# Performance work log

Measured on AMD Instinct MI355X. Metric: run time of the kernel, lower is better.

The kernel has to match this reference:

```python
import jax, jax.numpy as jnp
import numpy as np

KERNEL = 8


def setup_inputs() -> dict:
    key = jax.random.key(0)
    ks = jax.random.split(key, 9)
    N, Cin, L = 16, 128, 2048
    Cout = 256
    x = jax.random.normal(ks[0], (N, Cin, L), dtype=jnp.float32)
    conv_w = jax.random.normal(ks[1], (Cout, Cin, KERNEL), dtype=jnp.float32) * (1.0 / np.sqrt(Cin * KERNEL))
    conv_b = jax.random.normal(ks[2], (Cout,), dtype=jnp.float32) * 0.01
    wq = jax.random.normal(ks[3], (Cout, Cout), dtype=jnp.float32) * (1.0 / np.sqrt(Cout))
    bq = jax.random.normal(ks[4], (Cout,), dtype=jnp.float32) * 0.01
    wk = jax.random.normal(ks[5], (Cout, Cout), dtype=jnp.float32) * (1.0 / np.sqrt(Cout))
    bk = jax.random.normal(ks[6], (Cout,), dtype=jnp.float32) * 0.01
    wv = jax.random.normal(ks[7], (Cout, Cout), dtype=jnp.float32) * (1.0 / np.sqrt(Cout))
    bv = jax.random.normal(ks[8], (Cout,), dtype=jnp.float32) * 0.01
    return {"x": x, "conv_w": conv_w, "conv_b": conv_b,
            "wq": wq, "bq": bq, "wk": wk, "bk": bk, "wv": wv, "bv": bv}


def reference(x, conv_w, conv_b, wq, bq, wk, bk, wv, bv):
    # Conv1d, valid padding: [N, Cin, L] -> [N, Cout, S], S = L - KERNEL + 1
    h = jax.lax.conv_general_dilated(
        x, conv_w, window_strides=(1,), padding='VALID',
        dimension_numbers=('NCH', 'OIH', 'NCH'))
    h = jax.nn.relu(h + conv_b[None, :, None])
    N, C, S = h.shape
    h = jnp.transpose(h, (0, 2, 1))  # [N, S, C]
    # Linear layers (torch convention: y = x @ W^T + b)
    q = jnp.einsum('nsc,dc->nsd', h, wq) + bq
    k = jnp.einsum('nsc,dc->nsd', h, wk) + bk
    v = jnp.einsum('nsc,dc->nsd', h, wv) + bv
    # sigmoid (non-normalized) attention over full SxS scores
    scores = jnp.einsum('nsd,ntd->nst', q, k) / jnp.sqrt(jnp.asarray(C, h.dtype))
    attn = jax.nn.sigmoid(scores)  # [N, S, S]
    out = jnp.einsum('nst,ntd->nsd', attn, v)
    return jnp.transpose(out, (0, 2, 1))  # [N, C, S]
```

## Files before the change

kernel.cpp:

```cpp
#include <hip/hip_runtime.h>

typedef short short8 __attribute__((ext_vector_type(8)));
typedef float f32x4 __attribute__((ext_vector_type(4)));
typedef float f32x16 __attribute__((ext_vector_type(16)));
typedef unsigned short u16x4 __attribute__((ext_vector_type(4)));

constexpr int NB = 16, CIN = 128, LIN = 2048, CO = 256;
constexpr int SL = 2041;
constexpr int MT = NB * SL;
constexpr int MP = 32768;
constexpr int XTS = 136;

constexpr size_t XT_OFF = 0;
constexpr size_t XT_SZ  = (size_t)NB*LIN*XTS*2 + 65536;
constexpr size_t CW_OFF = XT_OFF + XT_SZ;
constexpr size_t CW_SZ  = (size_t)CO*CIN*8*2;
constexpr size_t WQ_OFF = CW_OFF + CW_SZ;
constexpr size_t WB_SZ  = (size_t)CO*CO*2;
constexpr size_t WK_OFF = WQ_OFF + WB_SZ;
constexpr size_t WV_OFF = WK_OFF + WB_SZ;
constexpr size_t H_OFF  = WV_OFF + WB_SZ;
constexpr size_t HB_SZ  = (size_t)MP*CO*2;
constexpr size_t Q_OFF  = H_OFF + HB_SZ;
constexpr size_t K_OFF  = Q_OFF + HB_SZ;
constexpr size_t VT_OFF = K_OFF + HB_SZ;

__device__ inline unsigned short f2bf(float f) {
  union { float f; unsigned int u; } v; v.f = f;
  unsigned int r = v.u + 0x7fffu + ((v.u >> 16) & 1u);
  return (unsigned short)(r >> 16);
}

#if defined(__has_builtin)
#if __has_builtin(__builtin_amdgcn_global_load_lds)
#define HAVE_GLDS 1
#endif
#endif

__device__ inline void gld16(const unsigned short* g, void* l) {
#ifdef HAVE_GLDS
  __builtin_amdgcn_global_load_lds(
      (const __attribute__((address_space(1))) void*)g,
      (__attribute__((address_space(3))) void*)l, 16, 0, 0);
#else
  *(short8*)l = *(const short8*)g;
#endif
}

__global__ void xpose_kernel(const float* __restrict__ x, unsigned short* __restrict__ xt) {
  __shared__ float tile[32][33];
  const int tx = threadIdx.x, ty = threadIdx.y;
  const int s0 = blockIdx.x * 32, c0 = blockIdx.y * 32, n = blockIdx.z;
  #pragma unroll
  for (int r = 0; r < 4; ++r)
    tile[ty * 4 + r][tx] = x[((size_t)(n * CIN + c0 + ty * 4 + r)) * LIN + s0 + tx];
  __syncthreads();
  #pragma unroll
  for (int r = 0; r < 4; ++r)
    xt[((size_t)(n * LIN + s0 + ty * 4 + r)) * XTS + c0 + tx] = f2bf(tile[tx][ty * 4 + r]);
}

__global__ void wconv_kernel(const float* __restrict__ w, unsigned short* __restrict__ o) {
  int idx = blockIdx.x * 256 + threadIdx.x;
  int co = idx >> 10, r = idx & 1023, kp = r >> 7, ci = r & 127;
  o[idx] = f2bf(w[co * 1024 + ci * 8 + kp]);
}

__global__ void wqkv_kernel(const float* __restrict__ a, const float* __restrict__ b,
                            const float* __restrict__ c, unsigned short* __restrict__ oa,
                            unsigned short* __restrict__ ob, unsigned short* __restrict__ oc) {
  int z = blockIdx.x >> 6, lb = blockIdx.x & 63;
  const float* src = (z == 0) ? a : (z == 1) ? b : c;
  unsigned short* dst = (z == 0) ? oa : (z == 1) ? ob : oc;
  int i = (lb * 256 + threadIdx.x) * 4;
  float4 v = *(const float4*)(src + i);
  u16x4 r;
  r.x = f2bf(v.x); r.y = f2bf(v.y); r.z = f2bf(v.z); r.w = f2bf(v.w);
  *(u16x4*)(dst + i) = r;
}

__global__ __launch_bounds__(256) void conv_gemm(
    const unsigned short* __restrict__ xt,
    const unsigned short* __restrict__ wb,
    const float* __restrict__ bias,
    unsigned short* __restrict__ h)
{
  __shared__ unsigned short sX[18432];
  __shared__ unsigned short sB[4096];
  const int tid = threadIdx.x;
  const int w = tid >> 6, lane = tid & 63, quad = lane >> 4, l16 = lane & 15;
  const int n  = blockIdx.y;
  const int s0 = blockIdx.x * 128;
  const int d0 = blockIdx.z * 128;

  {
    const unsigned short* xbase = xt + ((size_t)n * LIN + s0) * XTS;
    #pragma unroll
    for (int i = 0; i < 9; ++i) {
      int u = i * 256 + tid;
      gld16(xbase + u * 8, ((char*)sX) + u * 16);
    }
  }

  f32x4 acc[2][8];
  #pragma unroll
  for (int i = 0; i < 2; ++i)
    #pragma unroll
    for (int j = 0; j < 8; ++j) acc[i][j] = (f32x4){0.f, 0.f, 0.f, 0.f};

  for (int kc = 0; kc < 32; ++kc) {
    const int kp = kc >> 2, ci0 = (kc & 3) * 32;
    __syncthreads();
    #pragma unroll
    for (int i2 = 0; i2 < 2; ++i2) {
      int off = (i2 * 256 + tid) * 16;
      int row = off >> 6, kgs = (off >> 4) & 3;
      int kg = kgs ^ ((row >> 1) & 3);
      gld16(wb + (size_t)(d0 + row) * 1024 + kp * 128 + ci0 + kg * 8, ((char*)sB) + off);
    }
    __syncthreads();

    short8 bfr[8];
    #pragma unroll
    for (int j = 0; j < 8; ++j) {
      int r = j * 16 + l16;
      bfr[j] = *(const short8*)(sB + r * 32 + (quad ^ ((r >> 1) & 3)) * 8);
    }

    #pragma unroll
    for (int i = 0; i < 2; ++i) {
      int srow = w * 32 + i * 16 + l16;
      short8 afr = *(const short8*)(sX + (srow + kp) * XTS + ci0 + quad * 8);
      #pragma unroll
      for (int j = 0; j < 8; ++j)
        acc[i][j] = __builtin_amdgcn_mfma_f32_16x16x32_bf16(afr, bfr[j], acc[i][j], 0, 0, 0);
    }
  }

  #pragma unroll
  for (int i = 0; i < 2; ++i)
    #pragma unroll
    for (int j = 0; j < 8; ++j) {
      int col = d0 + j * 16 + l16;
      float bv = bias[col];
      #pragma unroll
      for (int jj = 0; jj < 4; ++jj) {
        int s = s0 + w * 32 + i * 16 + quad * 4 + jj;
        if (s < SL) {
          float val = fmaxf(acc[i][j][jj] + bv, 0.f);
          h[(size_t)(n * SL + s) * CO + col] = f2bf(val);
        }
      }
    }
}

__global__ __launch_bounds__(256) void lin_gemm(
    const unsigned short* __restrict__ A,
    const unsigned short* __restrict__ Bq, const unsigned short* __restrict__ Bk,
    const unsigned short* __restrict__ Bv,
    const float* __restrict__ biq, const float* __restrict__ bik,
    const float* __restrict__ biv,
    unsigned short* __restrict__ qb, unsigned short* __restrict__ kb,
    unsigned short* __restrict__ vtb)
{
  __shared__ unsigned short sA[4096];
  __shared__ unsigned short sB[4096];
  const int tid = threadIdx.x;
  const int w = tid >> 6, lane = tid & 63, quad = lane >> 4, l16 = lane & 15;
  const int m0 = blockIdx.x * 128, d0 = blockIdx.y * 128, z = blockIdx.z;
  const unsigned short* B = (z == 0) ? Bq : (z == 1) ? Bk : Bv;
  const float* bias        = (z == 0) ? biq : (z == 1) ? bik : biv;

  f32x4 acc[2][8];
  #pragma unroll
  for (int i = 0; i < 2; ++i)
    #pragma unroll
    for (int j = 0; j < 8; ++j) acc[i][j] = (f32x4){0.f, 0.f, 0.f, 0.f};

  for (int kc = 0; kc < 8; ++kc) {
    __syncthreads();
    #pragma unroll
    for (int i2 = 0; i2 < 2; ++i2) {
      int off = (i2 * 256 + tid) * 16;
      int row = off >> 6, kgs = (off >> 4) & 3;
      int kg = kgs ^ ((row >> 1) & 3);
      gld16(A + (size_t)(m0 + row) * CO + kc * 32 + kg * 8, ((char*)sA) + off);
      gld16(B + (size_t)(d0 + row) * CO + kc * 32 + kg * 8, ((char*)sB) + off);
    }
    __syncthreads();

    short8 afr[2], bfr[8];
    #pragma unroll
    for (int i = 0; i < 2; ++i) {
      int r = w * 32 + i * 16 + l16;
      afr[i] = *(const short8*)(sA + r * 32 + (quad ^ ((r >> 1) & 3)) * 8);
    }
    #pragma unroll
    for (int j = 0; j < 8; ++j) {
      int r = j * 16 + l16;
      bfr[j] = *(const short8*)(sB + r * 32 + (quad ^ ((r >> 1) & 3)) * 8);
    }
    #pragma unroll
    for (int i = 0; i < 2; ++i)
      #pragma unroll
      for (int j = 0; j < 8; ++j)
        acc[i][j] = __builtin_amdgcn_mfma_f32_16x16x32_bf16(afr[i], bfr[j], acc[i][j], 0, 0, 0);
  }

  #pragma unroll
  for (int i = 0; i < 2; ++i)
    #pragma unroll
    for (int j = 0; j < 8; ++j) {
      int col = d0 + j * 16 + l16;
      float bv = bias[col];
      #pragma unroll
      for (int jj = 0; jj < 4; ++jj) {
        int m = m0 + w * 32 + i * 16 + quad * 4 + jj;
        float val = acc[i][j][jj] + bv;
        if (z < 2) {
          ((z == 0) ? qb : kb)[(size_t)m * CO + col] = f2bf(val);
        } else if (m < MT) {
          int nn = m / SL, ss = m - nn * SL;
          vtb[(size_t)col * MP + nn * 2048 + ss] = f2bf(val);
        }
      }
    }
}

__global__ __launch_bounds__(256) void attn_kernel(
    const unsigned short* __restrict__ qb,
    const unsigned short* __restrict__ kb,
    const unsigned short* __restrict__ vtb,
    float* __restrict__ out)
{
  __shared__ char smem[40960];
  unsigned short* sKV = (unsigned short*)smem;
  unsigned short* sP  = (unsigned short*)(smem + 32768);
  const int tid = threadIdx.x;
  const int w = tid >> 6, lane = tid & 63;
  const int half = lane >> 5, l32 = lane & 31;
  const int n = blockIdx.y, s0 = blockIdx.x * 64;
  const int mi = w & 1, wh = w >> 1;

  short8 qf[16];
  {
    const unsigned short* qp =
        qb + (size_t)(n * SL + s0 + mi * 32 + l32) * CO + half * 8;
    #pragma unroll
    for (int kk = 0; kk < 16; ++kk) qf[kk] = *(const short8*)(qp + kk * 16);
  }

  f32x16 o[4];
  #pragma unroll
  for (int di = 0; di < 4; ++di)
    #pragma unroll
    for (int r = 0; r < 16; ++r) o[di][r] = 0.f;

  for (int t0 = 0; t0 < 2048; t0 += 64) {
    __syncthreads();
    #pragma unroll
    for (int i = 0; i < 8; ++i) {
      int u = i * 256 + tid;
      int trow = u >> 5, slot = u & 31;
      gld16(kb + (size_t)(n * SL + t0 + trow) * CO + (slot ^ (trow & 31)) * 8,
            ((char*)sKV) + u * 16);
    }
    __syncthreads();

    f32x16 sacc;
    #pragma unroll
    for (int r = 0; r < 16; ++r) sacc[r] = 0.f;
    const int tl = wh * 32 + l32;
    #pragma unroll
    for (int kk = 0; kk < 16; ++kk) {
      int g = kk * 2 + half;
      short8 kf = *(const short8*)(sKV + tl * 256 + (g ^ (tl & 31)) * 8);
      sacc = __builtin_amdgcn_mfma_f32_32x32x16_bf16(qf[kk], kf, sacc, 0, 0, 0);
    }

    #pragma unroll
    for (int r = 0; r < 16; ++r) {
      int srow = mi * 32 + (r & 3) + 8 * (r >> 2) + 4 * half;
      float p = 1.f / (1.f + __expf(-sacc[r] * 0.0625f));
      sP[srow * 64 + (((tl >> 3) ^ (srow & 7)) << 3) + (tl & 7)] =
          (t0 + tl < SL) ? f2bf(p) : (unsigned short)0;
    }
    __syncthreads();

    #pragma unroll
    for (int i = 0; i < 8; ++i) {
      int u = i * 256 + tid;
      int drow = u >> 3, slot = u & 7;
      gld16(vtb + (size_t)drow * MP + n * 2048 + t0 + (slot ^ (drow & 7)) * 8,
            ((char*)sKV) + u * 16);
    }
    __syncthreads();

    #pragma unroll
    for (int kt = 0; kt < 4; ++kt) {
      int gc = kt * 2 + half;
      int srow = mi * 32 + l32;
      short8 pa = *(const short8*)(sP + srow * 64 + ((gc ^ (srow & 7)) << 3));
      #pragma unroll
      for (int di = 0; di < 4; ++di) {
        int d = (wh * 4 + di) * 32 + l32;
        short8 vf = *(const short8*)(sKV + d * 64 + ((gc ^ (d & 7)) << 3));
        o[di] = __builtin_amdgcn_mfma_f32_32x32x16_bf16(pa, vf, o[di], 0, 0, 0);
      }
    }
  }

  #pragma unroll
  for (int di = 0; di < 4; ++di) {
    int d = (wh * 4 + di) * 32 + l32;
    float* op = out + (size_t)n * CO * SL + (size_t)d * SL;
    #pragma unroll
    for (int r = 0; r < 16; ++r) {
      int s = s0 + mi * 32 + (r & 3) + 8 * (r >> 2) + 4 * half;
      if (s < SL) op[s] = o[di][r];
    }
  }
}

extern "C" void kernel_launch(void* const* d_in, const int* in_sizes, int n_in,
                              void* d_out, int out_size, void* d_ws, size_t ws_size,
                              hipStream_t stream) {
  const float* x      = (const float*)d_in[0];
  const float* conv_w = (const float*)d_in[1];
  const float* conv_b = (const float*)d_in[2];
  const float* wq     = (const float*)d_in[3];
  const float* bq     = (const float*)d_in[4];
  const float* wk     = (const float*)d_in[5];
  const float* bk     = (const float*)d_in[6];
  const float* wv     = (const float*)d_in[7];
  const float* bv     = (const float*)d_in[8];

  char* ws = (char*)d_ws;
  unsigned short* xt  = (unsigned short*)(ws + XT_OFF);
  unsigned short* cw  = (unsigned short*)(ws + CW_OFF);
  unsigned short* wqb = (unsigned short*)(ws + WQ_OFF);
  unsigned short* wkb = (unsigned short*)(ws + WK_OFF);
  unsigned short* wvb = (unsigned short*)(ws + WV_OFF);
  unsigned short* hb  = (unsigned short*)(ws + H_OFF);
  unsigned short* qb  = (unsigned short*)(ws + Q_OFF);
  unsigned short* kb  = (unsigned short*)(ws + K_OFF);
  unsigned short* vtb = (unsigned short*)(ws + VT_OFF);

  hipLaunchKernelGGL(xpose_kernel, dim3(64, 4, 16), dim3(32, 8), 0, stream, x, xt);
  hipLaunchKernelGGL(wconv_kernel, dim3(1024), dim3(256), 0, stream, conv_w, cw);
  hipLaunchKernelGGL(wqkv_kernel,  dim3(192), dim3(256), 0, stream,
                     wq, wk, wv, wqb, wkb, wvb);
  hipLaunchKernelGGL(conv_gemm, dim3(16, 16, 2), dim3(256), 0, stream, xt, cw, conv_b, hb);
  hipLaunchKernelGGL(lin_gemm,  dim3(256, 2, 3), dim3(256), 0, stream,
                     hb, wqb, wkb, wvb, bq, bk, bv, qb, kb, vtb);
  hipLaunchKernelGGL(attn_kernel, dim3(32, 16), dim3(256), 0, stream,
                     qb, kb, vtb, (float*)d_out);
}
```

Baseline: 286.9 us.

## Restructure attention to 32-row tiles reading K and V directly from global

The attention kernel now processes 32 query rows per block instead of 64, with each wave computing its own 32 key columns of a 128-wide key tile. K and V fragments are loaded straight from global memory rather than staged through shared memory, so only the probability tile stays in LDS, and one of the two barriers per step is removed. The grid doubles and launch bounds request 4 blocks per CU to raise occupancy. The cost is no reuse of K/V across waves in LDS, so global and L2 traffic rises, including strided V loads.

```diff
diff --git a/kernel.cpp b/kernel.cpp
--- a/kernel.cpp
+++ b/kernel.cpp
@@ -227,97 +227,77 @@
     }
 }
 
-__global__ __launch_bounds__(256) void attn_kernel(
+__global__ __launch_bounds__(256, 4) void attn_kernel(
     const unsigned short* __restrict__ qb,
     const unsigned short* __restrict__ kb,
     const unsigned short* __restrict__ vtb,
     float* __restrict__ out)
 {
-  __shared__ char smem[40960];
-  unsigned short* sKV = (unsigned short*)smem;
-  unsigned short* sP  = (unsigned short*)(smem + 32768);
+  __shared__ unsigned short sP[32 * 128];
   const int tid = threadIdx.x;
   const int w = tid >> 6, lane = tid & 63;
   const int half = lane >> 5, l32 = lane & 31;
-  const int n = blockIdx.y, s0 = blockIdx.x * 64;
-  const int mi = w & 1, wh = w >> 1;
+  const int n = blockIdx.y, s0 = blockIdx.x * 32;
+  const int tl = w * 32 + l32;
 
   short8 qf[16];
   {
-    const unsigned short* qp =
-        qb + (size_t)(n * SL + s0 + mi * 32 + l32) * CO + half * 8;
+    const unsigned short* qp = qb + (size_t)(n * SL + s0 + l32) * CO + half * 8;
     #pragma unroll
     for (int kk = 0; kk < 16; ++kk) qf[kk] = *(const short8*)(qp + kk * 16);
   }
 
-  f32x16 o[4];
-  #pragma unroll
-  for (int di = 0; di < 4; ++di)
-    #pragma unroll
-    for (int r = 0; r < 16; ++r) o[di][r] = 0.f;
-
-  for (int t0 = 0; t0 < 2048; t0 += 64) {
-    __syncthreads();
-    #pragma unroll
-    for (int i = 0; i < 8; ++i) {
-      int u = i * 256 + tid;
-      int trow = u >> 5, slot = u & 31;
-      gld16(kb + (size_t)(n * SL + t0 + trow) * CO + (slot ^ (trow & 31)) * 8,
-            ((char*)sKV) + u * 16);
-    }
-    __syncthreads();
-
+  f32x16 o[2];
+  #pragma unroll
+  for (int dd = 0; dd < 2; ++dd)
+    #pragma unroll
+    for (int r = 0; r < 16; ++r) o[dd][r] = 0.f;
+
+  const unsigned short* kbase = kb + (size_t)(n * SL) * CO + half * 8;
+  const unsigned short* vbase = vtb + (size_t)n * 2048;
+
+  for (int t0 = 0; t0 < 2048; t0 += 128) {
+    const unsigned short* kp = kbase + (size_t)(t0 + tl) * CO;
     f32x16 sacc;
     #pragma unroll
     for (int r = 0; r < 16; ++r) sacc[r] = 0.f;
-    const int tl = wh * 32 + l32;
     #pragma unroll
     for (int kk = 0; kk < 16; ++kk) {
-      int g = kk * 2 + half;
-      short8 kf = *(const short8*)(sKV + tl * 256 + (g ^ (tl & 31)) * 8);
+      short8 kf = *(const short8*)(kp + kk * 16);
       sacc = __builtin_amdgcn_mfma_f32_32x32x16_bf16(qf[kk], kf, sacc, 0, 0, 0);
     }
 
+    __syncthreads();
     #pragma unroll
     for (int r = 0; r < 16; ++r) {
-      int srow = mi * 32 + (r & 3) + 8 * (r >> 2) + 4 * half;
+      int srow = (r & 3) + 8 * (r >> 2) + 4 * half;
       float p = 1.f / (1.f + __expf(-sacc[r] * 0.0625f));
-      sP[srow * 64 + (((tl >> 3) ^ (srow & 7)) << 3) + (tl & 7)] =
+      sP[srow * 128 + (((tl >> 3) ^ (srow & 15)) << 3) + (tl & 7)] =
           (t0 + tl < SL) ? f2bf(p) : (unsigned short)0;
     }
     __syncthreads();
 
     #pragma unroll
-    for (int i = 0; i < 8; ++i) {
-      int u = i * 256 + tid;
-      int drow = u >> 3, slot = u & 7;
-      gld16(vtb + (size_t)drow * MP + n * 2048 + t0 + (slot ^ (drow & 7)) * 8,
-            ((char*)sKV) + u * 16);
-    }
-    __syncthreads();
-
-    #pragma unroll
-    for (int kt = 0; kt < 4; ++kt) {
-      int gc = kt * 2 + half;
-      int srow = mi * 32 + l32;
-      short8 pa = *(const short8*)(sP + srow * 64 + ((gc ^ (srow & 7)) << 3));
-      #pragma unroll
-      for (int di = 0; di < 4; ++di) {
-        int d = (wh * 4 + di) * 32 + l32;
-        short8 vf = *(const short8*)(sKV + d * 64 + ((gc ^ (d & 7)) << 3));
-        o[di] = __builtin_amdgcn_mfma_f32_32x32x16_bf16(pa, vf, o[di], 0, 0, 0);
+    for (int kt = 0; kt < 8; ++kt) {
+      int g = kt * 2 + half;
+      short8 pa = *(const short8*)(sP + l32 * 128 + ((g ^ (l32 & 15)) << 3));
+      #pragma unroll
+      for (int dd = 0; dd < 2; ++dd) {
+        int d = (w * 2 + dd) * 32 + l32;
+        short8 vf = *(const short8*)(vbase + (size_t)d * MP + t0 + g * 8);
+        o[dd] = __builtin_amdgcn_mfma_f32_32x32x16_bf16(pa, vf, o[dd], 0, 0, 0);
       }
     }
   }
 
   #pragma unroll
-  for (int di = 0; di < 4; ++di) {
-    int d = (wh * 4 + di) * 32 + l32;
+  for (int dd = 0; dd < 2; ++dd) {
+    int d = (w * 2 + dd) * 32 + l32;
     float* op = out + (size_t)n * CO * SL + (size_t)d * SL;
     #pragma unroll
     for (int r = 0; r < 16; ++r) {
-      int s = s0 + mi * 32 + (r & 3) + 8 * (r >> 2) + 4 * half;
-      if (s < SL) op[s] = o[di][r];
+      int s = s0 + (r & 3) + 8 * (r >> 2) + 4 * half;
+      if (s < SL) op[s] = o[dd][r];
     }
   }
 }
@@ -353,6 +333,6 @@
   hipLaunchKernelGGL(conv_gemm, dim3(16, 16, 2), dim3(256), 0, stream, xt, cw, conv_b, hb);
   hipLaunchKernelGGL(lin_gemm,  dim3(256, 2, 3), dim3(256), 0, stream,
                      hb, wqb, wkb, wvb, bq, bk, bv, qb, kb, vtb);
-  hipLaunchKernelGGL(attn_kernel, dim3(32, 16), dim3(256), 0, stream,
+  hipLaunchKernelGGL(attn_kernel, dim3(64, 16), dim3(256), 0, stream,
                      qb, kb, vtb, (float*)d_out);
 }
```

Measured after the change: 488.6 us. 70.3% more time.

## Prefetch next tiles into registers with double-buffered LDS across GEMM and attention

Applied to the files above, without the earlier changes.

Replaces the direct global-to-LDS loads in conv_gemm, lin_gemm and attn_kernel with register prefetch of the next K/V or weight tile, issued before the current tile's MFMA work and written to LDS afterwards. The GEMMs double-buffer LDS so each k-step needs one barrier instead of two. Attention keeps separate K and V buffers, so it no longer reloads V after the scores, and it remaps the grid to a 1D index that groups batches, with launch_bounds(256,2). The cost is higher register pressure (attention holds 16 extra short8 registers on top of qf and the accumulators), and a custom waitcnt barrier replaces __syncthreads.

```diff
diff --git a/kernel.cpp b/kernel.cpp
--- a/kernel.cpp
+++ b/kernel.cpp
@@ -31,6 +31,13 @@
   return (unsigned short)(r >> 16);
 }
 
+__device__ inline void sync_lds() {
+  __asm__ volatile("" ::: "memory");
+  __builtin_amdgcn_s_waitcnt(0xc07f);
+  __builtin_amdgcn_s_barrier();
+  __asm__ volatile("" ::: "memory");
+}
+
 #if defined(__has_builtin)
 #if __has_builtin(__builtin_amdgcn_global_load_lds)
 #define HAVE_GLDS 1
@@ -86,7 +93,7 @@
     unsigned short* __restrict__ h)
 {
   __shared__ unsigned short sX[18432];
-  __shared__ unsigned short sB[4096];
+  __shared__ unsigned short sB[2][4096];
   const int tid = threadIdx.x;
   const int w = tid >> 6, lane = tid & 63, quad = lane >> 4, l16 = lane & 15;
   const int n  = blockIdx.y;
@@ -102,6 +109,19 @@
     }
   }
 
+  const int brow0 = tid >> 2, bkgs = tid & 3;
+  short8 breg[2];
+  #pragma unroll
+  for (int i2 = 0; i2 < 2; ++i2) {
+    int row = i2 * 64 + brow0;
+    int kg = bkgs ^ ((row >> 1) & 3);
+    breg[i2] = *(const short8*)(wb + (size_t)(d0 + row) * 1024 + 0 * 128 + 0 + kg * 8);
+  }
+  #pragma unroll
+  for (int i2 = 0; i2 < 2; ++i2)
+    *(short8*)(&sB[0][(i2 * 256 + tid) * 8]) = breg[i2];
+  __syncthreads();
+
   f32x4 acc[2][8];
   #pragma unroll
   for (int i = 0; i < 2; ++i)
@@ -109,24 +129,23 @@
     for (int j = 0; j < 8; ++j) acc[i][j] = (f32x4){0.f, 0.f, 0.f, 0.f};
 
   for (int kc = 0; kc < 32; ++kc) {
+    const int kcn = (kc < 31) ? kc + 1 : kc;
+    const int kpn = kcn >> 2, ci0n = (kcn & 3) * 32;
+    #pragma unroll
+    for (int i2 = 0; i2 < 2; ++i2) {
+      int row = i2 * 64 + brow0;
+      int kg = bkgs ^ ((row >> 1) & 3);
+      breg[i2] = *(const short8*)(wb + (size_t)(d0 + row) * 1024 + kpn * 128 + ci0n + kg * 8);
+    }
+
     const int kp = kc >> 2, ci0 = (kc & 3) * 32;
-    __syncthreads();
-    #pragma unroll
-    for (int i2 = 0; i2 < 2; ++i2) {
-      int off = (i2 * 256 + tid) * 16;
-      int row = off >> 6, kgs = (off >> 4) & 3;
-      int kg = kgs ^ ((row >> 1) & 3);
-      gld16(wb + (size_t)(d0 + row) * 1024 + kp * 128 + ci0 + kg * 8, ((char*)sB) + off);
-    }
-    __syncthreads();
-
+    const unsigned short* sBc = sB[kc & 1];
     short8 bfr[8];
     #pragma unroll
     for (int j = 0; j < 8; ++j) {
       int r = j * 16 + l16;
-      bfr[j] = *(const short8*)(sB + r * 32 + (quad ^ ((r >> 1) & 3)) * 8);
-    }
-
+      bfr[j] = *(const short8*)(sBc + r * 32 + (quad ^ ((r >> 1) & 3)) * 8);
+    }
     #pragma unroll
     for (int i = 0; i < 2; ++i) {
       int srow = w * 32 + i * 16 + l16;
@@ -135,6 +154,11 @@
       for (int j = 0; j < 8; ++j)
         acc[i][j] = __builtin_amdgcn_mfma_f32_16x16x32_bf16(afr, bfr[j], acc[i][j], 0, 0, 0);
     }
+
+    #pragma unroll
+    for (int i2 = 0; i2 < 2; ++i2)
+      *(short8*)(&sB[(kc + 1) & 1][(i2 * 256 + tid) * 8]) = breg[i2];
+    sync_lds();
   }
 
   #pragma unroll
@@ -163,14 +187,30 @@
     unsigned short* __restrict__ qb, unsigned short* __restrict__ kb,
     unsigned short* __restrict__ vtb)
 {
-  __shared__ unsigned short sA[4096];
-  __shared__ unsigned short sB[4096];
+  __shared__ unsigned short sA[2][4096];
+  __shared__ unsigned short sB[2][4096];
   const int tid = threadIdx.x;
   const int w = tid >> 6, lane = tid & 63, quad = lane >> 4, l16 = lane & 15;
   const int m0 = blockIdx.x * 128, d0 = blockIdx.y * 128, z = blockIdx.z;
   const unsigned short* B = (z == 0) ? Bq : (z == 1) ? Bk : Bv;
   const float* bias        = (z == 0) ? biq : (z == 1) ? bik : biv;
 
+  const int brow0 = tid >> 2, bkgs = tid & 3;
+  short8 areg[2], breg[2];
+  #pragma unroll
+  for (int i2 = 0; i2 < 2; ++i2) {
+    int row = i2 * 64 + brow0;
+    int kg = bkgs ^ ((row >> 1) & 3);
+    areg[i2] = *(const short8*)(A + (size_t)(m0 + row) * CO + kg * 8);
+    breg[i2] = *(const short8*)(B + (size_t)(d0 + row) * CO + kg * 8);
+  }
+  #pragma unroll
+  for (int i2 = 0; i2 < 2; ++i2) {
+    *(short8*)(&sA[0][(i2 * 256 + tid) * 8]) = areg[i2];
+    *(short8*)(&sB[0][(i2 * 256 + tid) * 8]) = breg[i2];
+  }
+  sync_lds();
+
   f32x4 acc[2][8];
   #pragma unroll
   for (int i = 0; i < 2; ++i)
@@ -178,33 +218,40 @@
     for (int j = 0; j < 8; ++j) acc[i][j] = (f32x4){0.f, 0.f, 0.f, 0.f};
 
   for (int kc = 0; kc < 8; ++kc) {
-    __syncthreads();
+    const int kcn = (kc < 7) ? kc + 1 : kc;
     #pragma unroll
     for (int i2 = 0; i2 < 2; ++i2) {
-      int off = (i2 * 256 + tid) * 16;
-      int row = off >> 6, kgs = (off >> 4) & 3;
-      int kg = kgs ^ ((row >> 1) & 3);
-      gld16(A + (size_t)(m0 + row) * CO + kc * 32 + kg * 8, ((char*)sA) + off);
-      gld16(B + (size_t)(d0 + row) * CO + kc * 32 + kg * 8, ((char*)sB) + off);
-    }
-    __syncthreads();
-
+      int row = i2 * 64 + brow0;
+      int kg = bkgs ^ ((row >> 1) & 3);
+      areg[i2] = *(const short8*)(A + (size_t)(m0 + row) * CO + kcn * 32 + kg * 8);
+      breg[i2] = *(const short8*)(B + (size_t)(d0 + row) * CO + kcn * 32 + kg * 8);
+    }
+
+    const unsigned short* sAc = sA[kc & 1];
+    const unsigned short* sBc = sB[kc & 1];
     short8 afr[2], bfr[8];
     #pragma unroll
     for (int i = 0; i < 2; ++i) {
       int r = w * 32 + i * 16 + l16;
-      afr[i] = *(const short8*)(sA + r * 32 + (quad ^ ((r >> 1) & 3)) * 8);
+      afr[i] = *(const short8*)(sAc + r * 32 + (quad ^ ((r >> 1) & 3)) * 8);
     }
     #pragma unroll
     for (int j = 0; j < 8; ++j) {
       int r = j * 16 + l16;
-      bfr[j] = *(const short8*)(sB + r * 32 + (quad ^ ((r >> 1) & 3)) * 8);
+      bfr[j] = *(const short8*)(sBc + r * 32 + (quad ^ ((r >> 1) & 3)) * 8);
     }
     #pragma unroll
     for (int i = 0; i < 2; ++i)
       #pragma unroll
       for (int j = 0; j < 8; ++j)
         acc[i][j] = __builtin_amdgcn_mfma_f32_16x16x32_bf16(afr[i], bfr[j], acc[i][j], 0, 0, 0);
+
+    #pragma unroll
+    for (int i2 = 0; i2 < 2; ++i2) {
+      *(short8*)(&sA[(kc + 1) & 1][(i2 * 256 + tid) * 8]) = areg[i2];
+      *(short8*)(&sB[(kc + 1) & 1][(i2 * 256 + tid) * 8]) = breg[i2];
+    }
+    sync_lds();
   }
 
   #pragma unroll
@@ -227,54 +274,75 @@
     }
 }
 
-__global__ __launch_bounds__(256) void attn_kernel(
+__global__ __launch_bounds__(256, 2) void attn_kernel(
     const unsigned short* __restrict__ qb,
     const unsigned short* __restrict__ kb,
     const unsigned short* __restrict__ vtb,
     float* __restrict__ out)
 {
-  __shared__ char smem[40960];
-  unsigned short* sKV = (unsigned short*)smem;
-  unsigned short* sP  = (unsigned short*)(smem + 32768);
+  __shared__ unsigned short sK[16384];
+  __shared__ unsigned short sV[16384];
+  __shared__ unsigned short sP[4096];
   const int tid = threadIdx.x;
   const int w = tid >> 6, lane = tid & 63;
   const int half = lane >> 5, l32 = lane & 31;
-  const int n = blockIdx.y, s0 = blockIdx.x * 64;
+  const int bidx = blockIdx.x;
+  const int n = (bidx & 7) + ((bidx >> 8) << 3);
+  const int s0 = ((bidx >> 3) & 31) * 64;
   const int mi = w & 1, wh = w >> 1;
+  const int tl = wh * 32 + l32;
+
+  const int ktrow = tid >> 5, kslot = tid & 31;
+  const int vdrow = tid >> 3, vslot = tid & 7;
 
   short8 qf[16];
   {
-    const unsigned short* qp =
-        qb + (size_t)(n * SL + s0 + mi * 32 + l32) * CO + half * 8;
+    const unsigned short* qp = qb + (size_t)(n * SL + s0 + mi * 32 + l32) * CO + half * 8;
     #pragma unroll
     for (int kk = 0; kk < 16; ++kk) qf[kk] = *(const short8*)(qp + kk * 16);
   }
 
+  const unsigned short* kbN = kb + (size_t)(n * SL) * CO;
+  const unsigned short* vbN = vtb + (size_t)n * 2048;
+
+  short8 kreg[8], vreg[8];
+  #pragma unroll
+  for (int i = 0; i < 8; ++i) {
+    int trow = i * 8 + ktrow;
+    kreg[i] = *(const short8*)(kbN + (size_t)trow * CO + ((kslot ^ (trow & 31)) << 3));
+    int drow = i * 32 + vdrow;
+    vreg[i] = *(const short8*)(vbN + (size_t)drow * MP + ((vslot ^ (drow & 7)) << 3));
+  }
+  #pragma unroll
+  for (int i = 0; i < 8; ++i) {
+    *(short8*)(sK + (i * 256 + tid) * 8) = kreg[i];
+    *(short8*)(sV + (i * 256 + tid) * 8) = vreg[i];
+  }
+  sync_lds();
+
   f32x16 o[4];
   #pragma unroll
   for (int di = 0; di < 4; ++di)
     #pragma unroll
     for (int r = 0; r < 16; ++r) o[di][r] = 0.f;
 
-  for (int t0 = 0; t0 < 2048; t0 += 64) {
-    __syncthreads();
+  for (int it = 0; it < 32; ++it) {
+    const int t0 = it * 64;
+    const int tn = (it < 31) ? t0 + 64 : t0;
     #pragma unroll
     for (int i = 0; i < 8; ++i) {
-      int u = i * 256 + tid;
-      int trow = u >> 5, slot = u & 31;
-      gld16(kb + (size_t)(n * SL + t0 + trow) * CO + (slot ^ (trow & 31)) * 8,
-            ((char*)sKV) + u * 16);
-    }
-    __syncthreads();
+      int trow = i * 8 + ktrow;
+      kreg[i] = *(const short8*)(kbN + (size_t)(tn + trow) * CO + ((kslot ^ (trow & 31)) << 3));
+      int drow = i * 32 + vdrow;
+      vreg[i] = *(const short8*)(vbN + (size_t)drow * MP + tn + ((vslot ^ (drow & 7)) << 3));
+    }
 
     f32x16 sacc;
     #pragma unroll
     for (int r = 0; r < 16; ++r) sacc[r] = 0.f;
-    const int tl = wh * 32 + l32;
     #pragma unroll
     for (int kk = 0; kk < 16; ++kk) {
-      int g = kk * 2 + half;
-      short8 kf = *(const short8*)(sKV + tl * 256 + (g ^ (tl & 31)) * 8);
+      short8 kf = *(const short8*)(sK + tl * 256 + (((kk * 2 + half) ^ (tl & 31)) << 3));
       sacc = __builtin_amdgcn_mfma_f32_32x32x16_bf16(qf[kk], kf, sacc, 0, 0, 0);
     }
 
@@ -285,29 +353,28 @@
       sP[srow * 64 + (((tl >> 3) ^ (srow & 7)) << 3) + (tl & 7)] =
           (t0 + tl < SL) ? f2bf(p) : (unsigned short)0;
     }
-    __syncthreads();
-
-    #pragma unroll
-    for (int i = 0; i < 8; ++i) {
-      int u = i * 256 + tid;
-      int drow = u >> 3, slot = u & 7;
-      gld16(vtb + (size_t)drow * MP + n * 2048 + t0 + (slot ^ (drow & 7)) * 8,
-            ((char*)sKV) + u * 16);
-    }
-    __syncthreads();
+    sync_lds();
 
     #pragma unroll
     for (int kt = 0; kt < 4; ++kt) {
-      int gc = kt * 2 + half;
+      int g2 = kt * 2 + half;
       int srow = mi * 32 + l32;
-      short8 pa = *(const short8*)(sP + srow * 64 + ((gc ^ (srow & 7)) << 3));
+      short8 pa = *(const short8*)(sP + srow * 64 + ((g2 ^ (srow & 7)) << 3));
       #pragma unroll
       for (int di = 0; di < 4; ++di) {
         int d = (wh * 4 + di) * 32 + l32;
-        short8 vf = *(const short8*)(sKV + d * 64 + ((gc ^ (d & 7)) << 3));
+        short8 vf = *(const short8*)(sV + d * 64 + ((g2 ^ (d & 7)) << 3));
         o[di] = __builtin_amdgcn_mfma_f32_32x32x16_bf16(pa, vf, o[di], 0, 0, 0);
       }
     }
+    sync_lds();
+
+    #pragma unroll
+    for (int i = 0; i < 8; ++i) {
+      *(short8*)(sK + (i * 256 + tid) * 8) = kreg[i];
+      *(short8*)(sV + (i * 256 + tid) * 8) = vreg[i];
+    }
+    sync_lds();
   }
 
   #pragma unroll
@@ -353,6 +420,6 @@
   hipLaunchKernelGGL(conv_gemm, dim3(16, 16, 2), dim3(256), 0, stream, xt, cw, conv_b, hb);
   hipLaunchKernelGGL(lin_gemm,  dim3(256, 2, 3), dim3(256), 0, stream,
                      hb, wqb, wkb, wvb, bq, bk, bv, qb, kb, vtb);
-  hipLaunchKernelGGL(attn_kernel, dim3(32, 16), dim3(256), 0, stream,
+  hipLaunchKernelGGL(attn_kernel, dim3(512), dim3(256), 0, stream,
                      qb, kb, vtb, (float*)d_out);
 }
```

Result: slower. 325.8 us (+13.5%).
